# Kernel tuning notes

Hardware: AMD Instinct MI355X
Metric: run time of the kernel (lower is better)

## Reference

```python
import jax, jax.numpy as jnp
import numpy as np

EPS = 1e-7

# ---- Poincare ball (c=1) manifold ops ----

def _logmap0(y):
    n = jnp.linalg.norm(y, axis=-1, keepdims=True)
    n = jnp.clip(n, EPS, 1.0 - 1e-5)
    return jnp.arctanh(n) * y / n


def _expmap0(v):
    n = jnp.maximum(jnp.linalg.norm(v, axis=-1, keepdims=True), EPS)
    return jnp.tanh(n) * v / n


def _pair_dist(q):
    # q: [B,N,H,D] points in the Poincare ball.
    # d(x,y) = arccosh(1 + 2||x-y||^2 / ((1-||x||^2)(1-||y||^2)))  (== 2 artanh ||(-x)+_m y||)
    sq = jnp.sum(q * q, axis=-1)                       # [B,N,H]
    dot = jnp.einsum('bnhd,bmhd->bnmh', q, q)          # [B,N,N,H] (batched GEMM)
    diff = jnp.maximum(sq[:, :, None, :] + sq[:, None, :, :] - 2.0 * dot, 0.0)
    denom = jnp.maximum((1.0 - sq[:, :, None, :]) * (1.0 - sq[:, None, :, :]), EPS)
    return jnp.arccosh(jnp.maximum(1.0 + 2.0 * diff / denom, 1.0 + EPS))  # [B,N,N,H]


def _hgat(x, adj, W, a_src, a_dst, multihead):
    # Hyperbolic GAT layer: log-map to tangent at origin, per-head linear +
    # masked GAT attention, exp-map back. use_act=False, no bias.
    xt = _logmap0(x)                                   # [B,N,Din]
    h = jnp.einsum('bnd,hde->bnhe', xt, W)             # [B,N,H,D]
    es = jnp.einsum('bnhe,he->bnh', h, a_src)
    ed = jnp.einsum('bnhe,he->bnh', h, a_dst)
    e = jax.nn.leaky_relu(es[:, :, None, :] + ed[:, None, :, :], 0.2)  # [B,N,N,H]
    e = jnp.where(adj[:, :, :, None] > 0, e, -1e9)
    att = jax.nn.softmax(e, axis=2)                    # over neighbors
    out = jnp.einsum('bnmh,bmhe->bnhe', att, h)        # [B,N,H,D]
    if multihead:
        return _expmap0(out)                           # per-head hyperbolic points
    B, N, H, D = out.shape
    return _expmap0(out.reshape(B, N, H * D))          # concat heads


def setup_inputs() -> dict:
    key = jax.random.key(0)
    B, N, DIN, DATT, DOUT, H = 8, 1024, 256, 64, 256, 4
    ks = jax.random.split(key, 8)
    x = _expmap0(0.5 * jax.random.normal(ks[0], (B, N, DIN), dtype=jnp.float32))
    a0 = (jax.random.uniform(ks[1], (B, N, N)) < 0.05).astype(jnp.float32)
    adj = jnp.maximum(a0, jnp.swapaxes(a0, -1, -2))
    adj = jnp.maximum(adj, jnp.eye(N, dtype=jnp.float32)[None])
    flags = jnp.ones((B, N), dtype=jnp.float32)
    s_in = 1.0 / np.sqrt(DIN)
    Wq = jax.random.normal(ks[2], (H, DIN, DATT), dtype=jnp.float32) * s_in
    aq_src = jax.random.normal(ks[3], (H, DATT), dtype=jnp.float32) / np.sqrt(DATT)
    aq_dst = jax.random.normal(ks[4], (H, DATT), dtype=jnp.float32) / np.sqrt(DATT)
    Dv = DOUT // H
    Wv = jax.random.normal(ks[5], (H, DIN, Dv), dtype=jnp.float32) * s_in
    av_src = jax.random.normal(ks[6], (H, Dv), dtype=jnp.float32) / np.sqrt(Dv)
    av_dst = jax.random.normal(ks[7], (H, Dv), dtype=jnp.float32) / np.sqrt(Dv)
    r = jnp.ones((H,), dtype=jnp.float32) * 5.0
    t = jnp.ones((H,), dtype=jnp.float32)
    return {"x": x, "adj": adj, "flags": flags, "Wq": Wq, "aq_src": aq_src,
            "aq_dst": aq_dst, "Wv": Wv, "av_src": av_src, "av_dst": av_dst,
            "r": r, "t": t}


def reference(x, adj, flags, Wq, aq_src, aq_dst, Wv, av_src, av_dst, r, t):
    B, N = adj.shape[0], adj.shape[1]
    query = _hgat(x, adj, Wq, aq_src, aq_dst, True)    # [B,N,H,DATT]
    value = _hgat(x, adj, Wv, av_src, av_dst, False)   # [B,N,DOUT]
    dist = _pair_dist(query)                           # [B,N,N,H]
    dist = dist.reshape(-1, B, N, N)                   # faithful torch .view(-1,*adj.shape)
    att = jnp.tanh((r[:, None, None, None] - dist) * t[:, None, None, None])
    att = att.reshape(-1, B, N, N).mean(axis=0)        # head-average -> [B,N,N]
    att = (att + jnp.swapaxes(att, -1, -2)) / 2.0      # symmetrize
    return value, att
```

## Files before the change

### kernel.cpp

```cpp
#include <hip/hip_runtime.h>
#include <hip/hip_bf16.h>
#include <math.h>

#define DEV __device__ __forceinline__

constexpr int B = 8, N = 1024, DIN = 256, H = 4, DATT = 64, DV = 64;
constexpr int BN = B * N;
constexpr int HD = H * DATT;
constexpr int HDV = H * DV;
constexpr int COLS = HD + HDV;
constexpr int BHN = B * H * N;
constexpr float EPSF = 1e-7f;

using short8 = __attribute__((ext_vector_type(8))) short;
using f32x4  = __attribute__((ext_vector_type(4))) float;

DEV unsigned short f2bf(float f) {
    __hip_bfloat16 h = __float2bfloat16(f);
    return *reinterpret_cast<unsigned short*>(&h);
}
DEV float bfu2f(unsigned short u) { return __uint_as_float(((unsigned)u) << 16); }

DEV void tsplit(float v, short& hs, short& ls) {
    unsigned vu = __float_as_uint(v);
    float lo = v - __uint_as_float(vu & 0xFFFF0000u);
    hs = (short)(unsigned short)(vu >> 16);
    ls = (short)(unsigned short)(__float_as_uint(lo) >> 16);
}

__global__ void k_scale(const float* __restrict__ x, float* __restrict__ s) {
    int p = blockIdx.x * 4 + (threadIdx.x >> 6);
    int l = threadIdx.x & 63;
    const float4* xr = reinterpret_cast<const float4*>(x + (size_t)p * DIN);
    float4 u = xr[l];
    float ss = u.x * u.x + u.y * u.y + u.z * u.z + u.w * u.w;
    for (int m = 32; m; m >>= 1) ss += __shfl_xor(ss, m);
    if (l == 0) {
        float n = sqrtf(ss);
        n = fminf(fmaxf(n, EPSF), 1.0f - 1e-5f);
        float at = 0.5f * __logf((1.f + n) / (1.f - n));
        s[p] = at / n;
    }
}

__global__ void k_wcat(const float* __restrict__ Wq, const float* __restrict__ Wv,
                       float* __restrict__ Wc) {
    int idx = blockIdx.x * 256 + threadIdx.x;
    int k = idx >> 9, c = idx & 511;
    int cc = c & 255;
    int h = cc >> 6, e = cc & 63;
    const float* src = (c < HD) ? Wq : Wv;
    Wc[idx] = src[(h * DIN + k) * 64 + e];
}

__global__ __launch_bounds__(256) void k_gemm(const float* __restrict__ x,
                                              const float* __restrict__ s,
                                              const float* __restrict__ Wc,
                                              float* __restrict__ hall) {
    __shared__ float As[16][68];
    __shared__ float Bs[16][68];
    int bm = blockIdx.x, bn = blockIdx.y;
    int tid = threadIdx.x;
    int ty = tid >> 4, tx = tid & 15;
    float acc[4][4] = {};
    int rowbase = bm * 64, colbase = bn * 64;
    int am = tid >> 2;
    int ak = (tid & 3) * 4;
    float sc = s[rowbase + am];
    for (int kt = 0; kt < DIN; kt += 16) {
        float4 u = *reinterpret_cast<const float4*>(x + (size_t)(rowbase + am) * DIN + kt + ak);
        As[ak + 0][am] = u.x * sc;
        As[ak + 1][am] = u.y * sc;
        As[ak + 2][am] = u.z * sc;
        As[ak + 3][am] = u.w * sc;
        int bk = tid >> 4, bc = (tid & 15) * 4;
        float4 w4 = *reinterpret_cast<const float4*>(Wc + (size_t)(kt + bk) * COLS + colbase + bc);
        *reinterpret_cast<float4*>(&Bs[bk][bc]) = w4;
        __syncthreads();
        for (int k = 0; k < 16; k++) {
            float4 a4 = *reinterpret_cast<const float4*>(&As[k][ty * 4]);
            float4 b4 = *reinterpret_cast<const float4*>(&Bs[k][tx * 4]);
            float av[4] = {a4.x, a4.y, a4.z, a4.w};
            float bv[4] = {b4.x, b4.y, b4.z, b4.w};
            for (int i = 0; i < 4; i++)
                for (int j = 0; j < 4; j++) acc[i][j] = fmaf(av[i], bv[j], acc[i][j]);
        }
        __syncthreads();
    }
    for (int i = 0; i < 4; i++) {
        float4 o = make_float4(acc[i][0], acc[i][1], acc[i][2], acc[i][3]);
        *reinterpret_cast<float4*>(hall + (size_t)(rowbase + ty * 4 + i) * COLS + colbase + tx * 4) = o;
    }
}

__global__ __launch_bounds__(256) void k_hT(const float* __restrict__ hall,
                                            unsigned short* __restrict__ hallT) {
    int jt = blockIdx.x, h = blockIdx.y, b = blockIdx.z;
    __shared__ float T[64][69];
    int t = threadIdx.x;
    int bh = b * H + h;
    int jl = t >> 2, cg = t & 3;
    int el = t >> 2, seg = t & 3;
    #pragma unroll
    for (int pass = 0; pass < 2; pass++) {
        int colbase = (pass == 0) ? h * 64 : 256 + h * 64;
        __syncthreads();
        {
            const float* src = hall + (size_t)(b * N + jt * 64 + jl) * COLS + colbase + cg * 16;
            #pragma unroll
            for (int u = 0; u < 4; u++) {
                float4 v = *reinterpret_cast<const float4*>(src + u * 4);
                T[jl][cg * 16 + u * 4 + 0] = v.x;
                T[jl][cg * 16 + u * 4 + 1] = v.y;
                T[jl][cg * 16 + u * 4 + 2] = v.z;
                T[jl][cg * 16 + u * 4 + 3] = v.w;
            }
        }
        __syncthreads();
        {
            unsigned int pk[8];
            #pragma unroll
            for (int k = 0; k < 8; k++) {
                float f0 = T[seg * 16 + 2 * k][el];
                float f1 = T[seg * 16 + 2 * k + 1][el];
                pk[k] = (unsigned)f2bf(f0) | ((unsigned)f2bf(f1) << 16);
            }
            unsigned short* dst = hallT + ((size_t)(bh * 128 + pass * 64 + el)) * 1024
                                  + jt * 64 + seg * 16;
            *reinterpret_cast<uint4*>(dst)     = make_uint4(pk[0], pk[1], pk[2], pk[3]);
            *reinterpret_cast<uint4*>(dst + 8) = make_uint4(pk[4], pk[5], pk[6], pk[7]);
        }
    }
}

__global__ void k_esed(const float* __restrict__ hall, const float* __restrict__ aqs,
                       const float* __restrict__ aqd, const float* __restrict__ avs,
                       const float* __restrict__ avd, float* __restrict__ esq,
                       float* __restrict__ edq, float* __restrict__ esv,
                       float* __restrict__ edv) {
    int p = blockIdx.x;
    int h = threadIdx.x >> 6, e = threadIdx.x & 63;
    float hq = hall[(size_t)p * COLS + h * 64 + e];
    float hv = hall[(size_t)p * COLS + 256 + h * 64 + e];
    float v1 = hq * aqs[h * 64 + e];
    float v2 = hq * aqd[h * 64 + e];
    float v3 = hv * avs[h * 64 + e];
    float v4 = hv * avd[h * 64 + e];
    for (int m = 32; m; m >>= 1) {
        v1 += __shfl_xor(v1, m); v2 += __shfl_xor(v2, m);
        v3 += __shfl_xor(v3, m); v4 += __shfl_xor(v4, m);
    }
    if (e == 0) {
        int b = p >> 10, n = p & 1023;
        int o = (b * H + h) * N + n;
        esq[o] = v1; edq[o] = v2; esv[o] = v3; edv[o] = v4;
    }
}

__global__ void k_stats(const float* __restrict__ adj, const float* __restrict__ esq,
                        const float* __restrict__ edq, const float* __restrict__ esv,
                        const float* __restrict__ edv, float* __restrict__ stats) {
    int bid = blockIdx.x;
    int i = bid & 1023;
    int bh = bid >> 10;
    int b = bh >> 2;
    int t = threadIdx.x;
    float esqi = esq[bid], esvi = esv[bid];
    const float* arow = adj + (size_t)(b * N + i) * N + t * 8;
    const float* edqr = edq + (size_t)bh * N + t * 8;
    const float* edvr = edv + (size_t)bh * N + t * 8;
    float4 a0 = *reinterpret_cast<const float4*>(arow);
    float4 a1 = *reinterpret_cast<const float4*>(arow + 4);
    float am[8] = {a0.x, a0.y, a0.z, a0.w, a1.x, a1.y, a1.z, a1.w};
    float4 q0 = *reinterpret_cast<const float4*>(edqr);
    float4 q1 = *reinterpret_cast<const float4*>(edqr + 4);
    float4 w0 = *reinterpret_cast<const float4*>(edvr);
    float4 w1 = *reinterpret_cast<const float4*>(edvr + 4);
    float edqv[8] = {q0.x, q0.y, q0.z, q0.w, q1.x, q1.y, q1.z, q1.w};
    float edvv[8] = {w0.x, w0.y, w0.z, w0.w, w1.x, w1.y, w1.z, w1.w};
    float eq[8], ev[8];
    float mq = -1e30f, mv = -1e30f;
    for (int j = 0; j < 8; j++) {
        bool msk = am[j] > 0.f;
        float q = esqi + edqv[j]; q = fmaxf(q, 0.2f * q);
        float v = esvi + edvv[j]; v = fmaxf(v, 0.2f * v);
        eq[j] = msk ? q : -1e30f;
        ev[j] = msk ? v : -1e30f;
        mq = fmaxf(mq, eq[j]); mv = fmaxf(mv, ev[j]);
    }
    __shared__ float red[2][2];
    __shared__ float red2[2][2];
    for (int m = 32; m; m >>= 1) { mq = fmaxf(mq, __shfl_xor(mq, m)); mv = fmaxf(mv, __shfl_xor(mv, m)); }
    int w = t >> 6;
    if ((t & 63) == 0) { red[w][0] = mq; red[w][1] = mv; }
    __syncthreads();
    mq = fmaxf(red[0][0], red[1][0]);
    mv = fmaxf(red[0][1], red[1][1]);
    float sq_ = 0.f, sv_ = 0.f;
    for (int j = 0; j < 8; j++) { sq_ += __expf(eq[j] - mq); sv_ += __expf(ev[j] - mv); }
    for (int m = 32; m; m >>= 1) { sq_ += __shfl_xor(sq_, m); sv_ += __shfl_xor(sv_, m); }
    if ((t & 63) == 0) { red2[w][0] = sq_; red2[w][1] = sv_; }
    __syncthreads();
    if (t == 0) {
        stats[bid] = mq;
        stats[BHN + bid] = red2[0][0] + red2[1][0];
        stats[2 * BHN + bid] = mv;
        stats[3 * BHN + bid] = red2[0][1] + red2[1][1];
    }
}

__global__ __launch_bounds__(512) void k_aggr(const float* __restrict__ adj,
        const unsigned short* __restrict__ hallT, const float* __restrict__ esq,
        const float* __restrict__ edq, const float* __restrict__ esv,
        const float* __restrict__ edv, const float* __restrict__ stats,
        float* __restrict__ outq, float* __restrict__ outv) {
    int f = blockIdx.x;
    int g = ((f & 7) << 7) | (f >> 3);
    int it = g & 31;
    int bh = g >> 5;
    int h = bh & 3, b = bh >> 2;
    int i0 = it * 32;
    int t = threadIdx.x;
    int lane = t & 63, wv = t >> 6;
    int team = wv >> 1;
    int mh = wv & 1;

    int i = i0 + mh * 16 + (lane & 15);
    int bi = bh * N + i;
    float esq_i = esq[bi], esv_i = esv[bi];
    float mq_i = stats[bi];           float isq_i = 1.f / stats[BHN + bi];
    float mv_i = stats[2 * BHN + bi]; float isv_i = 1.f / stats[3 * BHN + bi];
    const float* adjrow = adj + (size_t)(b * N + i) * N;
    const float* edqrow = edq + (size_t)bh * N;
    const float* edvrow = edv + (size_t)bh * N;
    int klo = lane >> 4;
    const unsigned short* bbq = hallT
        + ((size_t)(bh * 128 + (lane & 15))) * 1024 + klo * 8;
    const unsigned short* bbv = bbq + (size_t)64 * 1024;

    f32x4 accq[4] = {}, accv[4] = {};
    int jbase = team * 256;
    for (int jj = 0; jj < 8; jj++) {
        int j0 = jbase + jj * 32;
        float4 a0 = *reinterpret_cast<const float4*>(adjrow + j0 + klo * 8);
        float4 a1 = *reinterpret_cast<const float4*>(adjrow + j0 + klo * 8 + 4);
        float4 q0 = *reinterpret_cast<const float4*>(edqrow + j0 + klo * 8);
        float4 q1 = *reinterpret_cast<const float4*>(edqrow + j0 + klo * 8 + 4);
        float4 v0 = *reinterpret_cast<const float4*>(edvrow + j0 + klo * 8);
        float4 v1 = *reinterpret_cast<const float4*>(edvrow + j0 + klo * 8 + 4);
        float av[8] = {a0.x, a0.y, a0.z, a0.w, a1.x, a1.y, a1.z, a1.w};
        float eq[8] = {q0.x, q0.y, q0.z, q0.w, q1.x, q1.y, q1.z, q1.w};
        float ev[8] = {v0.x, v0.y, v0.z, v0.w, v1.x, v1.y, v1.z, v1.w};
        short8 afq, afv;
        #pragma unroll
        for (int u = 0; u < 8; u++) {
            bool on = av[u] > 0.f;
            float q = esq_i + eq[u]; q = fmaxf(q, 0.2f * q);
            float v = esv_i + ev[u]; v = fmaxf(v, 0.2f * v);
            float wq = on ? __expf(q - mq_i) * isq_i : 0.f;
            float wvv = on ? __expf(v - mv_i) * isv_i : 0.f;
            afq[u] = (short)f2bf(wq);
            afv[u] = (short)f2bf(wvv);
        }
        #pragma unroll
        for (int nt = 0; nt < 4; nt++) {
            short8 bq = *reinterpret_cast<const short8*>(bbq + j0 + nt * 16384);
            accq[nt] = __builtin_amdgcn_mfma_f32_16x16x32_bf16(afq, bq, accq[nt], 0, 0, 0);
            short8 bv = *reinterpret_cast<const short8*>(bbv + j0 + nt * 16384);
            accv[nt] = __builtin_amdgcn_mfma_f32_16x16x32_bf16(afv, bv, accv[nt], 0, 0, 0);
        }
    }

    __shared__ __align__(16) float red[8192];
    int slot = (team >> 1) * 2 + mh;
    float* buf = red + slot * 2048;
    __syncthreads();
    if (team & 1) {
        #pragma unroll
        for (int k = 0; k < 4; k++) {
            *reinterpret_cast<f32x4*>(&buf[(k * 64 + lane) * 4])       = accq[k];
            *reinterpret_cast<f32x4*>(&buf[((k + 4) * 64 + lane) * 4]) = accv[k];
        }
    }
    __syncthreads();
    if (!(team & 1)) {
        #pragma unroll
        for (int k = 0; k < 4; k++) {
            f32x4 pq = *reinterpret_cast<const f32x4*>(&buf[(k * 64 + lane) * 4]);
            f32x4 pv = *reinterpret_cast<const f32x4*>(&buf[((k + 4) * 64 + lane) * 4]);
            accq[k] += pq; accv[k] += pv;
        }
    }
    __syncthreads();
    if (team == 2) {
        float* d2 = red + mh * 2048;
        #pragma unroll
        for (int k = 0; k < 4; k++) {
            *reinterpret_cast<f32x4*>(&d2[(k * 64 + lane) * 4])       = accq[k];
            *reinterpret_cast<f32x4*>(&d2[((k + 4) * 64 + lane) * 4]) = accv[k];
        }
    }
    __syncthreads();
    if (team == 0) {
        float* s2 = red + mh * 2048;
        #pragma unroll
        for (int nt = 0; nt < 4; nt++) {
            f32x4 pq = *reinterpret_cast<const f32x4*>(&s2[(nt * 64 + lane) * 4]);
            f32x4 pv = *reinterpret_cast<const f32x4*>(&s2[((nt + 4) * 64 + lane) * 4]);
            #pragma unroll
            for (int r = 0; r < 4; r++) {
                int irow = i0 + mh * 16 + (lane >> 4) * 4 + r;
                int e = nt * 16 + (lane & 15);
                outq[(size_t)(b * N + irow) * 256 + h * 64 + e] = accq[nt][r] + pq[r];
                outv[(size_t)(b * N + irow) * 256 + h * 64 + e] = accv[nt][r] + pv[r];
            }
        }
    }
}

__global__ void k_expmap(const float* __restrict__ outq, const float* __restrict__ outv,
                         unsigned short* __restrict__ qh, unsigned short* __restrict__ ql,
                         float* __restrict__ sq, float* __restrict__ isr,
                         float* __restrict__ val) {
    int p = blockIdx.x, t = threadIdx.x;
    int h = t >> 6, e = t & 63;
    float v = outq[(size_t)p * HD + t];
    float ss = v * v;
    for (int m = 32; m; m >>= 1) ss += __shfl_xor(ss, m);
    float n = fmaxf(sqrtf(ss), EPSF);
    float tn = tanhf(n);
    float qv = v * (tn / n);
    short hs, ls; tsplit(qv, hs, ls);
    qh[((size_t)p << 8) + t] = (unsigned short)hs;
    ql[((size_t)p << 8) + t] = (unsigned short)ls;
    if (e == 0) {
        float s = tn * tn;
        sq[h * BN + p] = s;
        isr[h * BN + p] = __builtin_amdgcn_rcpf(1.f - s);
    }

    float vv = outv[(size_t)p * HDV + t];
    float s2 = vv * vv;
    for (int m = 32; m; m >>= 1) s2 += __shfl_xor(s2, m);
    __shared__ float part[4];
    if (e == 0) part[h] = s2;
    __syncthreads();
    float tot = part[0] + part[1] + part[2] + part[3];
    float nv = fmaxf(sqrtf(tot), EPSF);
    float sclv = tanhf(nv) / nv;
    val[(size_t)p * HDV + t] = vv * sclv;
}

__global__ __launch_bounds__(256) void k_att(const unsigned short* __restrict__ qh,
        const unsigned short* __restrict__ ql, const float* __restrict__ sq,
        const float* __restrict__ isr, const float* __restrict__ rr,
        const float* __restrict__ tt, float* __restrict__ m_out) {
    int f = blockIdx.x;
    int g = ((f & 7) << 7) | (f >> 3);
    int b2 = g >> 7;
    int rem = g & 127;
    int c = rem >> 5, h = (rem >> 3) & 3, kc = (rem >> 1) & 3, xh = rem & 1;
    int t = threadIdx.x;
    int l = t & 63, w = t >> 6;
    int klo = l >> 4;

    int nstart = (b2 * 256 + kc * 64) & 1023;
    int mstart = c * 256 + xh * 128;

    float tacc[8][4] = {};

    #pragma unroll
    for (int a = 0; a < 4; a++) {
        int b = 2 * a + (b2 >> 2);
        size_t xbase = ((size_t)(b * N + nstart + w * 16 + (l & 15)) << 8) + h * 64 + klo * 8;
        short8 Ah[2], Al[2];
        #pragma unroll
        for (int kk = 0; kk < 2; kk++) {
            Ah[kk] = *reinterpret_cast<const short8*>(qh + xbase + kk * 32);
            Al[kk] = *reinterpret_cast<const short8*>(ql + xbase + kk * 32);
        }
        float ra = rr[a], ta = tt[a];
        float c1 = 2.f * ta;
        float c0 = c1 * ra * 1.44269504f;
        float sxr[4], ixr[4];
        #pragma unroll
        for (int r = 0; r < 4; r++) {
            int gx = h * BN + b * N + nstart + w * 16 + (l >> 4) * 4 + r;
            sxr[r] = sq[gx];
            ixr[r] = 2.f * isr[gx];
        }
        size_t ybase = ((size_t)(b * N + mstart + (l & 15)) << 8) + h * 64 + klo * 8;
        #pragma unroll
        for (int nt = 0; nt < 8; nt++) {
            size_t yb = ybase + ((size_t)(nt * 16) << 8);
            f32x4 acc = {};
            #pragma unroll
            for (int kk = 0; kk < 2; kk++) {
                short8 Bh = *reinterpret_cast<const short8*>(qh + yb + kk * 32);
                short8 Bl = *reinterpret_cast<const short8*>(ql + yb + kk * 32);
                acc = __builtin_amdgcn_mfma_f32_16x16x32_bf16(Ah[kk], Bh, acc, 0, 0, 0);
                acc = __builtin_amdgcn_mfma_f32_16x16x32_bf16(Ah[kk], Bl, acc, 0, 0, 0);
                acc = __builtin_amdgcn_mfma_f32_16x16x32_bf16(Al[kk], Bh, acc, 0, 0, 0);
            }
            int gy = h * BN + b * N + mstart + nt * 16 + (l & 15);
            float sy = sq[gy];
            float iy = isr[gy];
            #pragma unroll
            for (int r = 0; r < 4; r++) {
                float diff = fmaxf(fmaf(-2.f, acc[r], sxr[r] + sy), 0.f);
                float ixy = fminf(ixr[r] * iy, 2e7f);
                float z = fmaxf(fmaf(diff, ixy, 1.f), 1.f + EPSF);
                float s_ = z + __builtin_amdgcn_sqrtf(fmaf(z, z, -1.f));
                float l2 = __builtin_amdgcn_logf(s_);
                float ex = __builtin_amdgcn_exp2f(fmaf(-c1, l2, c0));
                float rc = __builtin_amdgcn_rcpf(ex + 1.f);
                tacc[nt][r] += fmaf(-2.f, rc, 1.f);
            }
        }
    }
    #pragma unroll
    for (int nt = 0; nt < 8; nt++) {
        #pragma unroll
        for (int r = 0; r < 4; r++) {
            int n_local = w * 16 + (l >> 4) * 4 + r;
            int n2 = c + 4 * (kc * 64 + n_local);
            int mloc = xh * 128 + nt * 16 + (l & 15);
            int m2 = 4 * mloc + h;
            m_out[((size_t)b2 << 20) + ((size_t)n2 << 10) + m2] = 0.25f * tacc[nt][r];
        }
    }
}

__global__ void k_sym(float* __restrict__ m) {
    int ti = blockIdx.x, tj = blockIdx.y, b = blockIdx.z;
    if (ti > tj) return;
    __shared__ float A[32][33], Bt[32][33];
    int t = threadIdx.x;
    int r = t >> 3, c4 = (t & 7) * 4;
    size_t baseA = ((size_t)b << 20) + (size_t)(ti * 32) * N + tj * 32;
    size_t baseB = ((size_t)b << 20) + (size_t)(tj * 32) * N + ti * 32;
    float4 ua = *reinterpret_cast<const float4*>(m + baseA + (size_t)r * N + c4);
    float4 ub = *reinterpret_cast<const float4*>(m + baseB + (size_t)r * N + c4);
    A[r][c4 + 0] = ua.x; A[r][c4 + 1] = ua.y; A[r][c4 + 2] = ua.z; A[r][c4 + 3] = ua.w;
    Bt[r][c4 + 0] = ub.x; Bt[r][c4 + 1] = ub.y; Bt[r][c4 + 2] = ub.z; Bt[r][c4 + 3] = ub.w;
    __syncthreads();
    for (int u = 0; u < 4; u++) {
        int cc = c4 + u;
        float oa = 0.5f * (A[r][cc] + Bt[cc][r]);
        float ob = 0.5f * (Bt[r][cc] + A[cc][r]);
        m[baseA + (size_t)r * N + cc] = oa;
        m[baseB + (size_t)r * N + cc] = ob;
    }
}

extern "C" void kernel_launch(void* const* d_in, const int* in_sizes, int n_in,
                              void* d_out, int out_size, void* d_ws, size_t ws_size,
                              hipStream_t stream) {
    const float* x   = (const float*)d_in[0];
    const float* adj = (const float*)d_in[1];
    const float* Wq  = (const float*)d_in[3];
    const float* aqs = (const float*)d_in[4];
    const float* aqd = (const float*)d_in[5];
    const float* Wv  = (const float*)d_in[6];
    const float* avs = (const float*)d_in[7];
    const float* avd = (const float*)d_in[8];
    const float* rr  = (const float*)d_in[9];
    const float* tt  = (const float*)d_in[10];

    float* ws = (float*)d_ws;
    float* s     = ws;
    float* Wc    = s + BN;
    float* hall  = Wc + 256 * COLS;
    float* esq   = hall + (size_t)BN * COLS;
    float* edq   = esq + BHN;
    float* esv   = edq + BHN;
    float* edv   = esv + BHN;
    float* stats = edv + BHN;
    float* outq  = stats + 4 * BHN;
    float* outv  = outq + (size_t)BN * HD;
    float* sq    = outv + (size_t)BN * HDV;
    unsigned short* hallT = (unsigned short*)(sq + H * BN);
    size_t need = (size_t)((char*)(hallT + (size_t)BN * COLS) - (char*)ws);
    if (ws_size < need) return;

    unsigned short* qh = (unsigned short*)hall;
    unsigned short* ql = qh + (size_t)BN * 256;
    float* isr = (float*)(ql + (size_t)BN * 256);

    float* val  = (float*)d_out;
    float* matt = (float*)d_out + (size_t)BN * HDV;

    k_scale<<<BN / 4, 256, 0, stream>>>(x, s);
    k_wcat<<<(256 * COLS) / 256, 256, 0, stream>>>(Wq, Wv, Wc);
    k_gemm<<<dim3(BN / 64, COLS / 64), 256, 0, stream>>>(x, s, Wc, hall);
    k_hT<<<dim3(16, H, B), 256, 0, stream>>>(hall, hallT);
    k_esed<<<BN, 256, 0, stream>>>(hall, aqs, aqd, avs, avd, esq, edq, esv, edv);
    k_stats<<<BHN, 128, 0, stream>>>(adj, esq, edq, esv, edv, stats);
    k_aggr<<<1024, 512, 0, stream>>>(adj, hallT, esq, edq, esv, edv, stats, outq, outv);
    k_expmap<<<BN, 256, 0, stream>>>(outq, outv, qh, ql, sq, isr, val);
    k_att<<<1024, 256, 0, stream>>>(qh, ql, sq, isr, rr, tt, matt);
    k_sym<<<dim3(32, 32, 8), 256, 0, stream>>>(matt);
}
```

Before: 263.0 us.

## Move projection GEMM to split-bf16 MFMA and reorder aggregation block mapping

Replaces the scalar fp32 LDS-tiled projection GEMM with an MFMA bf16 GEMM. Inputs are split into high and low bf16 parts in a new prep kernel, and three MFMA products are used to approximate fp32 accuracy. The weight concat kernel now writes a transposed split layout. It also changes the block-to-(b,h,tile) mapping in the aggregation kernel so the four heads of one tile are adjacent, which should improve adj reuse in cache. The cost is an extra prep pass and some loss of precision from the split.

```diff
diff --git a/kernel.cpp b/kernel.cpp
--- a/kernel.cpp
+++ b/kernel.cpp
@@ -43,54 +43,57 @@
     }
 }
 
+__global__ void k_prep(const float* __restrict__ x, const float* __restrict__ s,
+                       unsigned short* __restrict__ xsh, unsigned short* __restrict__ xsl) {
+    int p = blockIdx.x, t = threadIdx.x;
+    float v = x[((size_t)p << 8) + t] * s[p];
+    short hs, ls; tsplit(v, hs, ls);
+    xsh[((size_t)p << 8) + t] = (unsigned short)hs;
+    xsl[((size_t)p << 8) + t] = (unsigned short)ls;
+}
+
 __global__ void k_wcat(const float* __restrict__ Wq, const float* __restrict__ Wv,
-                       float* __restrict__ Wc) {
+                       unsigned short* __restrict__ wth, unsigned short* __restrict__ wtl) {
     int idx = blockIdx.x * 256 + threadIdx.x;
-    int k = idx >> 9, c = idx & 511;
-    int cc = c & 255;
-    int h = cc >> 6, e = cc & 63;
-    const float* src = (c < HD) ? Wq : Wv;
-    Wc[idx] = src[(h * DIN + k) * 64 + e];
-}
-
-__global__ __launch_bounds__(256) void k_gemm(const float* __restrict__ x,
-                                              const float* __restrict__ s,
-                                              const float* __restrict__ Wc,
-                                              float* __restrict__ hall) {
-    __shared__ float As[16][68];
-    __shared__ float Bs[16][68];
+    int c = idx >> 8, k = idx & 255;
+    int cc = c & 255, h = cc >> 6, e = cc & 63;
+    const float* src = (c < 256) ? Wq : Wv;
+    float v = src[(h * DIN + k) * 64 + e];
+    short hs, ls; tsplit(v, hs, ls);
+    wth[idx] = (unsigned short)hs;
+    wtl[idx] = (unsigned short)ls;
+}
+
+__global__ __launch_bounds__(256) void k_gemm(const unsigned short* __restrict__ xsh,
+        const unsigned short* __restrict__ xsl, const unsigned short* __restrict__ wth,
+        const unsigned short* __restrict__ wtl, float* __restrict__ hall) {
     int bm = blockIdx.x, bn = blockIdx.y;
-    int tid = threadIdx.x;
-    int ty = tid >> 4, tx = tid & 15;
-    float acc[4][4] = {};
-    int rowbase = bm * 64, colbase = bn * 64;
-    int am = tid >> 2;
-    int ak = (tid & 3) * 4;
-    float sc = s[rowbase + am];
-    for (int kt = 0; kt < DIN; kt += 16) {
-        float4 u = *reinterpret_cast<const float4*>(x + (size_t)(rowbase + am) * DIN + kt + ak);
-        As[ak + 0][am] = u.x * sc;
-        As[ak + 1][am] = u.y * sc;
-        As[ak + 2][am] = u.z * sc;
-        As[ak + 3][am] = u.w * sc;
-        int bk = tid >> 4, bc = (tid & 15) * 4;
-        float4 w4 = *reinterpret_cast<const float4*>(Wc + (size_t)(kt + bk) * COLS + colbase + bc);
-        *reinterpret_cast<float4*>(&Bs[bk][bc]) = w4;
-        __syncthreads();
-        for (int k = 0; k < 16; k++) {
-            float4 a4 = *reinterpret_cast<const float4*>(&As[k][ty * 4]);
-            float4 b4 = *reinterpret_cast<const float4*>(&Bs[k][tx * 4]);
-            float av[4] = {a4.x, a4.y, a4.z, a4.w};
-            float bv[4] = {b4.x, b4.y, b4.z, b4.w};
-            for (int i = 0; i < 4; i++)
-                for (int j = 0; j < 4; j++) acc[i][j] = fmaf(av[i], bv[j], acc[i][j]);
-        }
-        __syncthreads();
-    }
-    for (int i = 0; i < 4; i++) {
-        float4 o = make_float4(acc[i][0], acc[i][1], acc[i][2], acc[i][3]);
-        *reinterpret_cast<float4*>(hall + (size_t)(rowbase + ty * 4 + i) * COLS + colbase + tx * 4) = o;
-    }
+    int t = threadIdx.x;
+    int l = t & 63, w = t >> 6;
+    int klo = l >> 4;
+    int rowbase = bm * 64 + w * 16;
+    int colbase = bn * 64;
+    f32x4 acc[4] = {};
+    size_t abase = ((size_t)(rowbase + (l & 15)) << 8) + klo * 8;
+    size_t bbase = ((size_t)(colbase + (l & 15)) << 8) + klo * 8;
+    for (int kt = 0; kt < 8; kt++) {
+        int k0 = kt * 32;
+        short8 Ah = *reinterpret_cast<const short8*>(xsh + abase + k0);
+        short8 Al = *reinterpret_cast<const short8*>(xsl + abase + k0);
+        #pragma unroll
+        for (int nt = 0; nt < 4; nt++) {
+            short8 Bh = *reinterpret_cast<const short8*>(wth + bbase + (nt << 12) + k0);
+            short8 Bl = *reinterpret_cast<const short8*>(wtl + bbase + (nt << 12) + k0);
+            acc[nt] = __builtin_amdgcn_mfma_f32_16x16x32_bf16(Ah, Bh, acc[nt], 0, 0, 0);
+            acc[nt] = __builtin_amdgcn_mfma_f32_16x16x32_bf16(Ah, Bl, acc[nt], 0, 0, 0);
+            acc[nt] = __builtin_amdgcn_mfma_f32_16x16x32_bf16(Al, Bh, acc[nt], 0, 0, 0);
+        }
+    }
+    #pragma unroll
+    for (int nt = 0; nt < 4; nt++)
+        #pragma unroll
+        for (int r = 0; r < 4; r++)
+            hall[(size_t)(rowbase + (l >> 4) * 4 + r) * COLS + colbase + nt * 16 + (l & 15)] = acc[nt][r];
 }
 
 __global__ __launch_bounds__(256) void k_hT(const float* __restrict__ hall,
@@ -216,9 +219,10 @@
         float* __restrict__ outq, float* __restrict__ outv) {
     int f = blockIdx.x;
     int g = ((f & 7) << 7) | (f >> 3);
-    int it = g & 31;
-    int bh = g >> 5;
-    int h = bh & 3, b = bh >> 2;
+    int b = g >> 7;
+    int it = (g >> 2) & 31;
+    int h = g & 3;
+    int bh = b * H + h;
     int i0 = it * 32;
     int t = threadIdx.x;
     int lane = t & 63, wv = t >> 6;
@@ -483,6 +487,10 @@
     size_t need = (size_t)((char*)(hallT + (size_t)BN * COLS) - (char*)ws);
     if (ws_size < need) return;
 
+    unsigned short* wth = (unsigned short*)Wc;
+    unsigned short* wtl = wth + (size_t)512 * 256;
+    unsigned short* xsh = (unsigned short*)outq;
+    unsigned short* xsl = xsh + (size_t)BN * 256;
     unsigned short* qh = (unsigned short*)hall;
     unsigned short* ql = qh + (size_t)BN * 256;
     float* isr = (float*)(ql + (size_t)BN * 256);
@@ -491,8 +499,9 @@
     float* matt = (float*)d_out + (size_t)BN * HDV;
 
     k_scale<<<BN / 4, 256, 0, stream>>>(x, s);
-    k_wcat<<<(256 * COLS) / 256, 256, 0, stream>>>(Wq, Wv, Wc);
-    k_gemm<<<dim3(BN / 64, COLS / 64), 256, 0, stream>>>(x, s, Wc, hall);
+    k_prep<<<BN, 256, 0, stream>>>(x, s, xsh, xsl);
+    k_wcat<<<(512 * 256) / 256, 256, 0, stream>>>(Wq, Wv, wth, wtl);
+    k_gemm<<<dim3(BN / 64, COLS / 64), 256, 0, stream>>>(xsh, xsl, wth, wtl, hall);
     k_hT<<<dim3(16, H, B), 256, 0, stream>>>(hall, hallT);
     k_esed<<<BN, 256, 0, stream>>>(hall, aqs, aqd, avs, avd, esq, edq, esv, edv);
     k_stats<<<BHN, 128, 0, stream>>>(adj, esq, edq, esv, edv, stats);
```

After: 276.9 us. 5.3% more time.

## Pack adjacency into bitmask once and use it in stats and aggregation

Applied to the files above, without the earlier changes.

Adds a kernel that compresses the float adjacency matrix into a 1-bit-per-entry mask using wave ballots. The stats and aggregation kernels then read mask bits instead of 32 MB of floats, and each of them previously re-read adj once per head. The aggregation block-to-work mapping is also reordered so heads of the same batch and row tile run close together, which should improve cache reuse of the mask. The cost is one extra full pass over adj plus a small mask buffer.

```diff
diff --git a/kernel.cpp b/kernel.cpp
--- a/kernel.cpp
+++ b/kernel.cpp
@@ -51,6 +51,21 @@
     int h = cc >> 6, e = cc & 63;
     const float* src = (c < HD) ? Wq : Wv;
     Wc[idx] = src[(h * DIN + k) * 64 + e];
+}
+
+__global__ void k_pack(const float* __restrict__ adj, unsigned long long* __restrict__ amask) {
+    int row = blockIdx.x;
+    int t = threadIdx.x;
+    int w = t >> 6, l = t & 63;
+    const float* arow = adj + (size_t)row * N;
+    unsigned long long* mrow = amask + (size_t)row * 16;
+    #pragma unroll
+    for (int s = 0; s < 4; s++) {
+        int seg = s * 4 + w;
+        float v = arow[seg * 64 + l];
+        unsigned long long m = __ballot(v > 0.f);
+        if (l == 0) mrow[seg] = m;
+    }
 }
 
 __global__ __launch_bounds__(256) void k_gemm(const float* __restrict__ x,
@@ -157,7 +172,8 @@
     }
 }
 
-__global__ void k_stats(const float* __restrict__ adj, const float* __restrict__ esq,
+__global__ void k_stats(const unsigned long long* __restrict__ amask,
+                        const float* __restrict__ esq,
                         const float* __restrict__ edq, const float* __restrict__ esv,
                         const float* __restrict__ edv, float* __restrict__ stats) {
     int bid = blockIdx.x;
@@ -166,12 +182,9 @@
     int b = bh >> 2;
     int t = threadIdx.x;
     float esqi = esq[bid], esvi = esv[bid];
-    const float* arow = adj + (size_t)(b * N + i) * N + t * 8;
+    unsigned mb = ((const unsigned char*)amask)[(size_t)(b * N + i) * 128 + t];
     const float* edqr = edq + (size_t)bh * N + t * 8;
     const float* edvr = edv + (size_t)bh * N + t * 8;
-    float4 a0 = *reinterpret_cast<const float4*>(arow);
-    float4 a1 = *reinterpret_cast<const float4*>(arow + 4);
-    float am[8] = {a0.x, a0.y, a0.z, a0.w, a1.x, a1.y, a1.z, a1.w};
     float4 q0 = *reinterpret_cast<const float4*>(edqr);
     float4 q1 = *reinterpret_cast<const float4*>(edqr + 4);
     float4 w0 = *reinterpret_cast<const float4*>(edvr);
@@ -181,7 +194,7 @@
     float eq[8], ev[8];
     float mq = -1e30f, mv = -1e30f;
     for (int j = 0; j < 8; j++) {
-        bool msk = am[j] > 0.f;
+        bool msk = (mb >> j) & 1;
         float q = esqi + edqv[j]; q = fmaxf(q, 0.2f * q);
         float v = esvi + edvv[j]; v = fmaxf(v, 0.2f * v);
         eq[j] = msk ? q : -1e30f;
@@ -209,16 +222,17 @@
     }
 }
 
-__global__ __launch_bounds__(512) void k_aggr(const float* __restrict__ adj,
+__global__ __launch_bounds__(512) void k_aggr(const unsigned long long* __restrict__ amask,
         const unsigned short* __restrict__ hallT, const float* __restrict__ esq,
         const float* __restrict__ edq, const float* __restrict__ esv,
         const float* __restrict__ edv, const float* __restrict__ stats,
         float* __restrict__ outq, float* __restrict__ outv) {
     int f = blockIdx.x;
     int g = ((f & 7) << 7) | (f >> 3);
-    int it = g & 31;
-    int bh = g >> 5;
-    int h = bh & 3, b = bh >> 2;
+    int b = g >> 7;
+    int it = (g >> 2) & 31;
+    int h = g & 3;
+    int bh = b * H + h;
     int i0 = it * 32;
     int t = threadIdx.x;
     int lane = t & 63, wv = t >> 6;
@@ -230,7 +244,7 @@
     float esq_i = esq[bi], esv_i = esv[bi];
     float mq_i = stats[bi];           float isq_i = 1.f / stats[BHN + bi];
     float mv_i = stats[2 * BHN + bi]; float isv_i = 1.f / stats[3 * BHN + bi];
-    const float* adjrow = adj + (size_t)(b * N + i) * N;
+    const unsigned char* mrow = (const unsigned char*)amask + (size_t)(b * N + i) * 128;
     const float* edqrow = edq + (size_t)bh * N;
     const float* edvrow = edv + (size_t)bh * N;
     int klo = lane >> 4;
@@ -242,19 +256,17 @@
     int jbase = team * 256;
     for (int jj = 0; jj < 8; jj++) {
         int j0 = jbase + jj * 32;
-        float4 a0 = *reinterpret_cast<const float4*>(adjrow + j0 + klo * 8);
-        float4 a1 = *reinterpret_cast<const float4*>(adjrow + j0 + klo * 8 + 4);
+        unsigned mword = *reinterpret_cast<const unsigned*>(mrow + (j0 >> 3));
         float4 q0 = *reinterpret_cast<const float4*>(edqrow + j0 + klo * 8);
         float4 q1 = *reinterpret_cast<const float4*>(edqrow + j0 + klo * 8 + 4);
         float4 v0 = *reinterpret_cast<const float4*>(edvrow + j0 + klo * 8);
         float4 v1 = *reinterpret_cast<const float4*>(edvrow + j0 + klo * 8 + 4);
-        float av[8] = {a0.x, a0.y, a0.z, a0.w, a1.x, a1.y, a1.z, a1.w};
         float eq[8] = {q0.x, q0.y, q0.z, q0.w, q1.x, q1.y, q1.z, q1.w};
         float ev[8] = {v0.x, v0.y, v0.z, v0.w, v1.x, v1.y, v1.z, v1.w};
         short8 afq, afv;
         #pragma unroll
         for (int u = 0; u < 8; u++) {
-            bool on = av[u] > 0.f;
+            bool on = (mword >> (klo * 8 + u)) & 1;
             float q = esq_i + eq[u]; q = fmaxf(q, 0.2f * q);
             float v = esv_i + ev[u]; v = fmaxf(v, 0.2f * v);
             float wq = on ? __expf(q - mq_i) * isq_i : 0.f;
@@ -480,7 +492,8 @@
     float* outv  = outq + (size_t)BN * HD;
     float* sq    = outv + (size_t)BN * HDV;
     unsigned short* hallT = (unsigned short*)(sq + H * BN);
-    size_t need = (size_t)((char*)(hallT + (size_t)BN * COLS) - (char*)ws);
+    unsigned long long* amask = (unsigned long long*)(hallT + (size_t)BN * COLS);
+    size_t need = (size_t)((char*)(amask + (size_t)BN * 16) - (char*)ws);
     if (ws_size < need) return;
 
     unsigned short* qh = (unsigned short*)hall;
@@ -492,11 +505,12 @@
 
     k_scale<<<BN / 4, 256, 0, stream>>>(x, s);
     k_wcat<<<(256 * COLS) / 256, 256, 0, stream>>>(Wq, Wv, Wc);
+    k_pack<<<BN, 256, 0, stream>>>(adj, amask);
     k_gemm<<<dim3(BN / 64, COLS / 64), 256, 0, stream>>>(x, s, Wc, hall);
     k_hT<<<dim3(16, H, B), 256, 0, stream>>>(hall, hallT);
     k_esed<<<BN, 256, 0, stream>>>(hall, aqs, aqd, avs, avd, esq, edq, esv, edv);
-    k_stats<<<BHN, 128, 0, stream>>>(adj, esq, edq, esv, edv, stats);
-    k_aggr<<<1024, 512, 0, stream>>>(adj, hallT, esq, edq, esv, edv, stats, outq, outv);
+    k_stats<<<BHN, 128, 0, stream>>>(amask, esq, edq, esv, edv, stats);
+    k_aggr<<<1024, 512, 0, stream>>>(amask, hallT, esq, edq, esv, edv, stats, outq, outv);
     k_expmap<<<BN, 256, 0, stream>>>(outq, outv, qh, ql, sq, isr, val);
     k_att<<<1024, 256, 0, stream>>>(qh, ql, sq, isr, rr, tt, matt);
     k_sym<<<dim3(32, 32, 8), 256, 0, stream>>>(matt);
```

Measured after the change: 264.2 us. No clear change (+0.4%).

## Pack adjacency into bitmask in stats kernel and reuse it in aggregation

Applied to the files above, without the earlier changes.

The stats kernel now also writes a packed 1-bit-per-neighbor adjacency mask (once per batch, from head 0), and the aggregation kernel reads that mask instead of the full float adjacency rows. The aggregation block order is also remapped so that the four heads of the same batch and row tile run next to each other. This cuts the adjacency traffic in aggregation by a large factor. It costs an extra small mask write and a workspace buffer.

```diff
diff --git a/kernel.cpp b/kernel.cpp
--- a/kernel.cpp
+++ b/kernel.cpp
@@ -159,7 +159,8 @@
 
 __global__ void k_stats(const float* __restrict__ adj, const float* __restrict__ esq,
                         const float* __restrict__ edq, const float* __restrict__ esv,
-                        const float* __restrict__ edv, float* __restrict__ stats) {
+                        const float* __restrict__ edv, float* __restrict__ stats,
+                        unsigned char* __restrict__ amask) {
     int bid = blockIdx.x;
     int i = bid & 1023;
     int bh = bid >> 10;
@@ -179,15 +180,19 @@
     float edqv[8] = {q0.x, q0.y, q0.z, q0.w, q1.x, q1.y, q1.z, q1.w};
     float edvv[8] = {w0.x, w0.y, w0.z, w0.w, w1.x, w1.y, w1.z, w1.w};
     float eq[8], ev[8];
+    unsigned mb = 0;
     float mq = -1e30f, mv = -1e30f;
     for (int j = 0; j < 8; j++) {
         bool msk = am[j] > 0.f;
+        mb |= (unsigned)msk << j;
         float q = esqi + edqv[j]; q = fmaxf(q, 0.2f * q);
         float v = esvi + edvv[j]; v = fmaxf(v, 0.2f * v);
         eq[j] = msk ? q : -1e30f;
         ev[j] = msk ? v : -1e30f;
         mq = fmaxf(mq, eq[j]); mv = fmaxf(mv, ev[j]);
     }
+    if ((bh & 3) == 0)
+        amask[(size_t)(b * N + i) * 128 + t] = (unsigned char)mb;
     __shared__ float red[2][2];
     __shared__ float red2[2][2];
     for (int m = 32; m; m >>= 1) { mq = fmaxf(mq, __shfl_xor(mq, m)); mv = fmaxf(mv, __shfl_xor(mv, m)); }
@@ -209,16 +214,17 @@
     }
 }
 
-__global__ __launch_bounds__(512) void k_aggr(const float* __restrict__ adj,
+__global__ __launch_bounds__(512) void k_aggr(const unsigned char* __restrict__ amask,
         const unsigned short* __restrict__ hallT, const float* __restrict__ esq,
         const float* __restrict__ edq, const float* __restrict__ esv,
         const float* __restrict__ edv, const float* __restrict__ stats,
         float* __restrict__ outq, float* __restrict__ outv) {
     int f = blockIdx.x;
     int g = ((f & 7) << 7) | (f >> 3);
-    int it = g & 31;
-    int bh = g >> 5;
-    int h = bh & 3, b = bh >> 2;
+    int b = g >> 7;
+    int it = (g >> 2) & 31;
+    int h = g & 3;
+    int bh = b * H + h;
     int i0 = it * 32;
     int t = threadIdx.x;
     int lane = t & 63, wv = t >> 6;
@@ -230,7 +236,7 @@
     float esq_i = esq[bi], esv_i = esv[bi];
     float mq_i = stats[bi];           float isq_i = 1.f / stats[BHN + bi];
     float mv_i = stats[2 * BHN + bi]; float isv_i = 1.f / stats[3 * BHN + bi];
-    const float* adjrow = adj + (size_t)(b * N + i) * N;
+    const unsigned char* mrow = amask + (size_t)(b * N + i) * 128;
     const float* edqrow = edq + (size_t)bh * N;
     const float* edvrow = edv + (size_t)bh * N;
     int klo = lane >> 4;
@@ -242,19 +248,17 @@
     int jbase = team * 256;
     for (int jj = 0; jj < 8; jj++) {
         int j0 = jbase + jj * 32;
-        float4 a0 = *reinterpret_cast<const float4*>(adjrow + j0 + klo * 8);
-        float4 a1 = *reinterpret_cast<const float4*>(adjrow + j0 + klo * 8 + 4);
+        unsigned mword = *reinterpret_cast<const unsigned*>(mrow + (j0 >> 3));
         float4 q0 = *reinterpret_cast<const float4*>(edqrow + j0 + klo * 8);
         float4 q1 = *reinterpret_cast<const float4*>(edqrow + j0 + klo * 8 + 4);
         float4 v0 = *reinterpret_cast<const float4*>(edvrow + j0 + klo * 8);
         float4 v1 = *reinterpret_cast<const float4*>(edvrow + j0 + klo * 8 + 4);
-        float av[8] = {a0.x, a0.y, a0.z, a0.w, a1.x, a1.y, a1.z, a1.w};
         float eq[8] = {q0.x, q0.y, q0.z, q0.w, q1.x, q1.y, q1.z, q1.w};
         float ev[8] = {v0.x, v0.y, v0.z, v0.w, v1.x, v1.y, v1.z, v1.w};
         short8 afq, afv;
         #pragma unroll
         for (int u = 0; u < 8; u++) {
-            bool on = av[u] > 0.f;
+            bool on = (mword >> (klo * 8 + u)) & 1;
             float q = esq_i + eq[u]; q = fmaxf(q, 0.2f * q);
             float v = esv_i + ev[u]; v = fmaxf(v, 0.2f * v);
             float wq = on ? __expf(q - mq_i) * isq_i : 0.f;
@@ -480,7 +484,8 @@
     float* outv  = outq + (size_t)BN * HD;
     float* sq    = outv + (size_t)BN * HDV;
     unsigned short* hallT = (unsigned short*)(sq + H * BN);
-    size_t need = (size_t)((char*)(hallT + (size_t)BN * COLS) - (char*)ws);
+    unsigned char* amask = (unsigned char*)(hallT + (size_t)BN * COLS);
+    size_t need = (size_t)((char*)(amask + (size_t)BN * 128) - (char*)ws);
     if (ws_size < need) return;
 
     unsigned short* qh = (unsigned short*)hall;
@@ -495,8 +500,8 @@
     k_gemm<<<dim3(BN / 64, COLS / 64), 256, 0, stream>>>(x, s, Wc, hall);
     k_hT<<<dim3(16, H, B), 256, 0, stream>>>(hall, hallT);
     k_esed<<<BN, 256, 0, stream>>>(hall, aqs, aqd, avs, avd, esq, edq, esv, edv);
-    k_stats<<<BHN, 128, 0, stream>>>(adj, esq, edq, esv, edv, stats);
-    k_aggr<<<1024, 512, 0, stream>>>(adj, hallT, esq, edq, esv, edv, stats, outq, outv);
+    k_stats<<<BHN, 128, 0, stream>>>(adj, esq, edq, esv, edv, stats, amask);
+    k_aggr<<<1024, 512, 0, stream>>>(amask, hallT, esq, edq, esv, edv, stats, outq, outv);
     k_expmap<<<BN, 256, 0, stream>>>(outq, outv, qh, ql, sq, isr, val);
     k_att<<<1024, 256, 0, stream>>>(qh, ql, sq, isr, rr, tt, matt);
     k_sym<<<dim3(32, 32, 8), 256, 0, stream>>>(matt);
```

New measurement: 257.8 us. -2.0%, faster.
